# Performance work log

Hardware: AMD Instinct MI355X
Metric: run time of the kernel (lower is better)

## Reference

```python
import jax, jax.numpy as jnp
import numpy as np

B, T, D = 2, 1024, 1024
H, DH = 16, 64          # d_head = d_model // n_heads
MAX_POS = 64


def setup_inputs() -> dict:
    key = jax.random.key(0)
    ks = jax.random.split(key, 11)
    s = 1.0 / np.sqrt(D)
    x = jax.random.normal(ks[0], (B, T, D), jnp.float32)
    Wq = jax.random.normal(ks[1], (D, D), jnp.float32) * s
    Wk = jax.random.normal(ks[2], (D, D), jnp.float32) * s
    Wv = jax.random.normal(ks[3], (D, D), jnp.float32) * s
    Wo = jax.random.normal(ks[4], (D, D), jnp.float32) * s
    bq = jnp.zeros((D,), jnp.float32)
    bk = jnp.zeros((D,), jnp.float32)
    bv = jnp.zeros((D,), jnp.float32)
    bo = jnp.zeros((D,), jnp.float32)
    pos_emb = jax.random.normal(ks[5], (H, MAX_POS, DH), jnp.float32) * 0.02
    causal_mask = jnp.triu(jnp.ones((T, T), bool), k=1)  # True = masked (j > i)
    return dict(x=x, Wq=Wq, bq=bq, Wk=Wk, bk=bk, Wv=Wv, bv=bv, Wo=Wo, bo=bo,
                pos_emb=pos_emb, causal_mask=causal_mask)


def reference(x, Wq, bq, Wk, bk, Wv, bv, Wo, bo, pos_emb, causal_mask):
    Bv, Tv, _ = x.shape
    scale = np.sqrt(DH).astype(np.float32)

    def proj(W, b):
        return (x @ W.T + b).reshape(Bv, Tv, H, DH).transpose(0, 2, 1, 3)  # (B,H,T,d)

    Q, K, V = proj(Wq, bq), proj(Wk, bk), proj(Wv, bv)

    qk = jnp.einsum('bhid,bhjd->bhij', Q, K)              # (B,H,T,T)
    gates = jax.nn.sigmoid(qk / scale)
    gates = jnp.where(causal_mask, 0.0, gates)
    cum = jnp.cumsum(gates, axis=-1)
    pos = cum[..., -1:] - cum                             # total - cumsum_left

    pos = jnp.clip(pos, 0.0, MAX_POS - 1.0)
    pos_floor = jnp.floor(pos)
    alpha = (pos - pos_floor)[..., None]                  # (B,H,T,T,1) -> broadcast
    fidx = pos_floor.astype(jnp.int32)
    cidx = jnp.clip(jnp.ceil(pos), 0, MAX_POS - 1).astype(jnp.int32)

    # q_i . PE_{i,j} via precomputed q.pos_emb table (same math, no (B,H,T,T,d) tensor)
    qpe_tab = jnp.einsum('bhid,hpd->bhip', Q, pos_emb)    # (B,H,T,MAX_POS)
    qpe_f = jnp.take_along_axis(qpe_tab, fidx, axis=-1)   # (B,H,T,T)
    qpe_c = jnp.take_along_axis(qpe_tab, cidx, axis=-1)
    q_pe = (1.0 - alpha[..., 0]) * qpe_f + alpha[..., 0] * qpe_c

    scores = (qk + q_pe) / scale
    scores = jnp.where(causal_mask, -jnp.inf, scores)
    attn = jax.nn.softmax(scores, axis=-1)

    out = jnp.einsum('bhij,bhjd->bhid', attn, V)
    out = out.transpose(0, 2, 1, 3).reshape(Bv, Tv, D)
    return out @ Wo.T + bo
```

## Files before the change

kernel.cpp:

```cpp
#include <hip/hip_runtime.h>
#include <math.h>

#define Tt 1024
#define Dd 1024
#define Hh 16
#define DHh 64
#define MAXPOS 64
#define BTt 2048

typedef short short8 __attribute__((ext_vector_type(8)));
typedef float floatx4 __attribute__((ext_vector_type(4)));

#define MFMA16 __builtin_amdgcn_mfma_f32_16x16x32_bf16

__device__ __forceinline__ unsigned short f2bf(float f) {
    unsigned u;
    __builtin_memcpy(&u, &f, 4);
    u = (u + 0x7FFFu + ((u >> 16) & 1u)) >> 16;
    return (unsigned short)u;
}
__device__ __forceinline__ float bf2fs(short s) {
    unsigned u = ((unsigned)(unsigned short)s) << 16;
    float f;
    __builtin_memcpy(&f, &u, 4);
    return f;
}
__device__ __forceinline__ float fsigm(float x) {
    return __builtin_amdgcn_rcpf(1.f + __expf(-x));
}
__device__ __forceinline__ void gl2lds16(const short* __restrict__ g, short* l) {
    __builtin_amdgcn_global_load_lds(
        (const __attribute__((address_space(1))) void*)g,
        (__attribute__((address_space(3))) void*)l,
        16, 0, 0);
}

__global__ __launch_bounds__(256) void conv_bf16(
    const float* __restrict__ x,  const float* __restrict__ W0,
    const float* __restrict__ W1, const float* __restrict__ W2,
    const float* __restrict__ W3,
    short* __restrict__ xb, short* __restrict__ w0b, short* __restrict__ w1b,
    short* __restrict__ w2b, short* __restrict__ w3b)
{
    const float* src; short* dst; int n;
    switch (blockIdx.y) {
        case 0:  src = x;  dst = xb;  n = BTt * Dd; break;
        case 1:  src = W0; dst = w0b; n = Dd * Dd;  break;
        case 2:  src = W1; dst = w1b; n = Dd * Dd;  break;
        case 3:  src = W2; dst = w2b; n = Dd * Dd;  break;
        default: src = W3; dst = w3b; n = Dd * Dd;  break;
    }
    int idx = (blockIdx.x * 256 + threadIdx.x) * 8;
    if (idx >= n) return;
    floatx4 a0 = *(const floatx4*)&src[idx];
    floatx4 a1 = *(const floatx4*)&src[idx + 4];
    short8 s;
    for (int e = 0; e < 4; ++e) {
        s[e]     = (short)f2bf(a0[e]);
        s[e + 4] = (short)f2bf(a1[e]);
    }
    *(short8*)&dst[idx] = s;
}

template <int MODE, int TMW>
__device__ __forceinline__ void gemm_body(const short* __restrict__ A,
                                          const short* __restrict__ W,
                                          const float* __restrict__ bias,
                                          void* __restrict__ Cout,
                                          int N, int K)
{
    __shared__ __align__(16) short Ash[2][TMW * 64 * 64];
    __shared__ __align__(16) short Bsh[2][64 * 64];
    const int t = threadIdx.x;
    const int lane = t & 63, wave = t >> 6;
    const int quad = lane >> 4, l16 = lane & 15;
    const int row0 = blockIdx.x * (TMW * 64), col0 = blockIdx.y * 64;

    const int g_r = lane >> 3, g_c = (lane & 7) * 8;

    floatx4 acc[TMW][4];
    for (int a = 0; a < TMW; ++a)
        for (int b2 = 0; b2 < 4; ++b2)
            acc[a][b2] = (floatx4){0.f, 0.f, 0.f, 0.f};

#define STAGE(buf, kb)                                                      \
    do {                                                                    \
        for (int i = 0; i < TMW * 2; ++i) {                                 \
            int rbase = (wave * (TMW * 2) + i) * 8;                         \
            gl2lds16(&A[(size_t)(row0 + rbase + g_r) * K + (kb) + g_c],     \
                     &Ash[buf][rbase * 64]);                                \
        }                                                                   \
        for (int i = 0; i < 2; ++i) {                                       \
            int rbase = (wave * 2 + i) * 8;                                 \
            gl2lds16(&W[(size_t)(col0 + rbase + g_r) * K + (kb) + g_c],     \
                     &Bsh[buf][rbase * 64]);                                \
        }                                                                   \
    } while (0)

    const int NT = K / 64;
    STAGE(0, 0);
    __syncthreads();
    for (int ts = 0; ts < NT; ++ts) {
        const int cur = ts & 1;
        if (ts + 1 < NT) STAGE(cur ^ 1, (ts + 1) * 64);
        for (int ks = 0; ks < 2; ++ks) {
            short8 af[TMW], bfr[4];
            for (int tm = 0; tm < TMW; ++tm)
                af[tm] = *(short8*)&Ash[cur][(wave * (TMW * 16) + tm * 16 + l16) * 64 + ks * 32 + quad * 8];
            for (int tn = 0; tn < 4; ++tn)
                bfr[tn] = *(short8*)&Bsh[cur][(tn * 16 + l16) * 64 + ks * 32 + quad * 8];
            for (int tm = 0; tm < TMW; ++tm)
                for (int tn = 0; tn < 4; ++tn)
                    acc[tm][tn] = MFMA16(af[tm], bfr[tn], acc[tm][tn], 0, 0, 0);
        }
        if (ts + 1 < NT) __syncthreads();
    }
#undef STAGE
    for (int tm = 0; tm < TMW; ++tm)
        for (int tn = 0; tn < 4; ++tn) {
            int col = col0 + tn * 16 + l16;
            float bv = bias[col];
            for (int r = 0; r < 4; ++r) {
                int row = row0 + wave * (TMW * 16) + tm * 16 + quad * 4 + r;
                float v = acc[tm][tn][r] + bv;
                if (MODE == 0) ((float*)Cout)[(size_t)row * N + col] = v;
                else           ((short*)Cout)[(size_t)row * N + col] = (short)f2bf(v);
            }
        }
}

__global__ __launch_bounds__(256) void gemm_qkv(
    const short* __restrict__ xb,
    const short* __restrict__ Wqb, const short* __restrict__ Wkb,
    const short* __restrict__ Wvb,
    const float* __restrict__ bq, const float* __restrict__ bk,
    const float* __restrict__ bv,
    short* __restrict__ Qb, short* __restrict__ Kb, short* __restrict__ Vrow)
{
    if (blockIdx.z == 0)      gemm_body<1, 2>(xb, Wqb, bq, Qb, Dd, Dd);
    else if (blockIdx.z == 1) gemm_body<1, 2>(xb, Wkb, bk, Kb, Dd, Dd);
    else                      gemm_body<1, 2>(xb, Wvb, bv, Vrow, Dd, Dd);
}

__global__ __launch_bounds__(256) void gemm_o(
    const short* __restrict__ A, const short* __restrict__ W,
    const float* __restrict__ bias, float* __restrict__ C)
{
    gemm_body<0, 1>(A, W, bias, C, Dd, Dd);
}

__global__ __launch_bounds__(256) void v_transpose(
    const short* __restrict__ Vrow, short* __restrict__ Vt)
{
    __shared__ __align__(16) short L[64 * 72];
    const int t = threadIdx.x;
    const int j0 = blockIdx.x * 64, d0 = blockIdx.y * 64, b = blockIdx.z;
    for (int s = 0; s < 2; ++s) {
        int c = t * 2 + s;
        int jr = c >> 3, c8 = c & 7;
        *(short8*)&L[jr * 72 + c8 * 8] =
            *(const short8*)&Vrow[((size_t)(b * Tt + j0 + jr)) * Dd + d0 + c8 * 8];
    }
    __syncthreads();
    for (int s = 0; s < 2; ++s) {
        int c = t * 2 + s;
        int dr = c >> 3, c8 = c & 7;
        short8 v;
        for (int e = 0; e < 8; ++e) v[e] = L[(c8 * 8 + e) * 72 + dr];
        *(short8*)&Vt[((size_t)(b * Dd + d0 + dr)) * Tt + j0 + c8 * 8] = v;
    }
}

__global__ __launch_bounds__(256) void cope_attn(
    const short* __restrict__ Q, const short* __restrict__ K,
    const short* __restrict__ Vt, const float* __restrict__ PE,
    short* __restrict__ AOb)
{
    const int h = blockIdx.y, b = blockIdx.z;
    const int t = threadIdx.x, lane = t & 63, wave = t >> 6;
    const int quad = lane >> 4, l16 = lane & 15;

    __shared__ __align__(16) short SldS[32 * 264];
    __shared__ __align__(16) short KV[128 * 72];
    __shared__ short qpeB[32 * 68];
    __shared__ float lrow[32];
    float* Sld = (float*)SldS;

    const float inv_scale = 0.125f;
    const int sr = t >> 3, ss = t & 7;

    for (int phase = 0; phase < 2; ++phase) {
        const int it = (phase == 0) ? (31 - (int)blockIdx.x) : (int)blockIdx.x;
        const int i0 = it * 32;
        const int irow = i0 + sr;

        short* QtS = SldS;
        {
            int r = t >> 3, c = t & 7;
            *(short8*)&QtS[r * 72 + c * 8] =
                *(const short8*)&Q[((size_t)(b * Tt + i0 + r)) * Dd + h * DHh + c * 8];
        }
        for (int e = 0; e < 16; ++e) {
            int idx = t + 256 * e;
            int p = idx >> 6, d = idx & 63;
            KV[p * 72 + d] = (short)f2bf(PE[((size_t)h * MAXPOS + p) * DHh + d]);
        }
        __syncthreads();

        short8 qa[2][2];
        for (int rb = 0; rb < 2; ++rb)
            for (int ks = 0; ks < 2; ++ks)
                qa[rb][ks] = *(short8*)&QtS[(rb * 16 + l16) * 72 + ks * 32 + quad * 8];

        {
            int mt = wave >> 1;
            int ntA = 2 * (wave & 1), ntB = ntA + 1;
            floatx4 c0f = {0, 0, 0, 0}, c1f = {0, 0, 0, 0};
            for (int ks = 0; ks < 2; ++ks) {
                short8 b0 = *(short8*)&KV[(ntA * 16 + l16) * 72 + ks * 32 + quad * 8];
                short8 b1 = *(short8*)&KV[(ntB * 16 + l16) * 72 + ks * 32 + quad * 8];
                c0f = MFMA16(qa[mt][ks], b0, c0f, 0, 0, 0);
                c1f = MFMA16(qa[mt][ks], b1, c1f, 0, 0, 0);
            }
            for (int r = 0; r < 4; ++r) {
                qpeB[(mt * 16 + quad * 4 + r) * 68 + ntA * 16 + l16] = (short)f2bf(c0f[r]);
                qpeB[(mt * 16 + quad * 4 + r) * 68 + ntB * 16 + l16] = (short)f2bf(c1f[r]);
            }
        }

        const int JT = (i0 + 159) >> 7;
        floatx4 o0 = {0, 0, 0, 0}, o1 = {0, 0, 0, 0};
        const int pv_mt = wave >> 1;
        const int pv_ntA = 2 * (wave & 1), pv_ntB = pv_ntA + 1;
        float l_acc = 0.f;
        float rightAcc = 0.f;

        short8 kreg[4];
        for (int e = 0; e < 4; ++e) {
            int ch = t + 256 * e;
            int jr = ch >> 3, c = ch & 7;
            kreg[e] = *(const short8*)&K[((size_t)(b * Tt + (JT - 1) * 128 + jr)) * Dd + h * DHh + c * 8];
        }

        for (int jt = JT - 1; jt >= 0; --jt) {
            const int j0 = jt * 128;
            __syncthreads();
            for (int e = 0; e < 4; ++e) {
                int ch = t + 256 * e;
                int jr = ch >> 3, c = ch & 7;
                *(short8*)&KV[jr * 72 + c * 8] = kreg[e];
            }
            __syncthreads();
            {
                int ntA = 2 * wave, ntB = ntA + 1;
                floatx4 c00 = {0,0,0,0}, c01 = {0,0,0,0}, c10 = {0,0,0,0}, c11 = {0,0,0,0};
                for (int ks = 0; ks < 2; ++ks) {
                    short8 b0 = *(short8*)&KV[(ntA * 16 + l16) * 72 + ks * 32 + quad * 8];
                    short8 b1 = *(short8*)&KV[(ntB * 16 + l16) * 72 + ks * 32 + quad * 8];
                    c00 = MFMA16(qa[0][ks], b0, c00, 0, 0, 0);
                    c01 = MFMA16(qa[0][ks], b1, c01, 0, 0, 0);
                    c10 = MFMA16(qa[1][ks], b0, c10, 0, 0, 0);
                    c11 = MFMA16(qa[1][ks], b1, c11, 0, 0, 0);
                }
                for (int r = 0; r < 4; ++r) {
                    Sld[(quad * 4 + r) * 132 + ntA * 16 + l16] = c00[r];
                    Sld[(quad * 4 + r) * 132 + ntB * 16 + l16] = c01[r];
                    Sld[(16 + quad * 4 + r) * 132 + ntA * 16 + l16] = c10[r];
                    Sld[(16 + quad * 4 + r) * 132 + ntB * 16 + l16] = c11[r];
                }
            }
            __syncthreads();
            short8 vreg[4];
            for (int e = 0; e < 4; ++e) {
                int ch = t + 256 * e;
                int d = ch >> 4, c = ch & 15;
                vreg[e] = *(const short8*)&Vt[((size_t)(b * Dd + h * DHh + d)) * Tt + j0 + c * 8];
            }
            if (jt > 0) {
                for (int e = 0; e < 4; ++e) {
                    int ch = t + 256 * e;
                    int jr = ch >> 3, c = ch & 7;
                    kreg[e] = *(const short8*)&K[((size_t)(b * Tt + j0 - 128 + jr)) * Dd + h * DHh + c * 8];
                }
            }
            {
                floatx4 qv[4];
                for (int q4 = 0; q4 < 4; ++q4) {
                    short8 qraw = *(short8*)&SldS[sr * 264 + ss * 32 + q4 * 8];
                    __builtin_memcpy(&qv[q4], &qraw, 16);
                }
                float gt[16];
                float gs = 0.f;
                for (int e = 0; e < 16; ++e) {
                    int j = j0 + ss * 16 + e;
                    float qk = qv[e >> 2][e & 3];
                    float g = (j <= irow) ? fsigm(qk * inv_scale) : 0.f;
                    gt[e] = g;
                    gs += g;
                }
                float inc = gs;
                for (int d2 = 1; d2 < 8; d2 <<= 1) {
                    float n = __shfl_down(inc, d2, 64);
                    if ((lane & 7) + d2 < 8) inc += n;
                }
                float tileTot = __shfl(inc, lane & 56, 64);
                float base = rightAcc + (inc - gs);
                float run = 0.f;
                short8 p0, p1;
                for (int e = 15; e >= 0; --e) {
                    int j = j0 + ss * 16 + e;
                    float pos = base + run;
                    run += gt[e];
                    pos = fminf(fmaxf(pos, 0.f), 63.f);
                    float pf = floorf(pos);
                    float al = pos - pf;
                    int fi = (int)pf;
                    int ci = fi + 1; if (ci > 63) ci = 63;
                    float qp = (1.f - al) * bf2fs(qpeB[sr * 68 + fi]) + al * bf2fs(qpeB[sr * 68 + ci]);
                    float qk = qv[e >> 2][e & 3];
                    float p = (j <= irow) ? __expf((qk + qp) * inv_scale) : 0.f;
                    if (e < 8) p0[e] = (short)f2bf(p); else p1[e - 8] = (short)f2bf(p);
                    l_acc += p;
                }
                *(short8*)&SldS[sr * 264 + ss * 32]     = p0;
                *(short8*)&SldS[sr * 264 + ss * 32 + 8] = p1;
                rightAcc += tileTot;
            }
            for (int e = 0; e < 4; ++e) {
                int ch = t + 256 * e;
                int d = ch >> 4, c = ch & 15;
                *(short8*)&KV[d * 136 + c * 8] = vreg[e];
            }
            __syncthreads();
            for (int ks = 0; ks < 4; ++ks) {
                short8 a  = *(short8*)&SldS[(pv_mt * 16 + l16) * 264 + ks * 64
                                            + ((quad >> 1) << 5) + ((quad & 1) << 3)];
                short8 b0 = *(short8*)&KV[(pv_ntA * 16 + l16) * 136 + ks * 32 + quad * 8];
                short8 b1 = *(short8*)&KV[(pv_ntB * 16 + l16) * 136 + ks * 32 + quad * 8];
                o0 = MFMA16(a, b0, o0, 0, 0, 0);
                o1 = MFMA16(a, b1, o1, 0, 0, 0);
            }
        }
        float lr = l_acc;
        for (int d2 = 4; d2 >= 1; d2 >>= 1) lr += __shfl_xor(lr, d2, 64);
        if (ss == 0) lrow[sr] = lr;
        __syncthreads();
        for (int r = 0; r < 4; ++r) {
            int row = pv_mt * 16 + quad * 4 + r;
            float inv = __builtin_amdgcn_rcpf(lrow[row]);
            size_t off = ((size_t)(b * Tt + i0 + row)) * Dd + h * DHh;
            AOb[off + pv_ntA * 16 + l16] = (short)f2bf(o0[r] * inv);
            AOb[off + pv_ntB * 16 + l16] = (short)f2bf(o1[r] * inv);
        }
    }
}

extern "C" void kernel_launch(void* const* d_in, const int* in_sizes, int n_in,
                              void* d_out, int out_size, void* d_ws, size_t ws_size,
                              hipStream_t stream)
{
    const float* x  = (const float*)d_in[0];
    const float* Wq = (const float*)d_in[1];
    const float* bq = (const float*)d_in[2];
    const float* Wk = (const float*)d_in[3];
    const float* bk = (const float*)d_in[4];
    const float* Wv = (const float*)d_in[5];
    const float* bv = (const float*)d_in[6];
    const float* Wo = (const float*)d_in[7];
    const float* bo = (const float*)d_in[8];
    const float* pe = (const float*)d_in[9];

    short* xb   = (short*)d_ws;
    short* Wqb  = xb   + (size_t)BTt * Dd;
    short* Wkb  = Wqb  + (size_t)Dd * Dd;
    short* Wvb  = Wkb  + (size_t)Dd * Dd;
    short* Wob  = Wvb  + (size_t)Dd * Dd;
    short* Qb   = Wob  + (size_t)Dd * Dd;
    short* Kb   = Qb   + (size_t)BTt * Dd;
    short* Vrow = Kb   + (size_t)BTt * Dd;
    short* Vtg  = Vrow + (size_t)BTt * Dd;
    short* AOb  = Vtg  + (size_t)BTt * Dd;

    dim3 gc(BTt * Dd / 8 / 256, 5);
    conv_bf16<<<gc, 256, 0, stream>>>(x, Wq, Wk, Wv, Wo, xb, Wqb, Wkb, Wvb, Wob);

    dim3 gq(BTt / 128, Dd / 64, 3);
    gemm_qkv<<<gq, 256, 0, stream>>>(xb, Wqb, Wkb, Wvb, bq, bk, bv, Qb, Kb, Vrow);

    dim3 gv(Tt / 64, Dd / 64, 2);
    v_transpose<<<gv, 256, 0, stream>>>(Vrow, Vtg);

    dim3 ga(Tt / 32 / 2, Hh, 2);
    cope_attn<<<ga, 256, 0, stream>>>(Qb, Kb, Vtg, pe, AOb);

    dim3 go(BTt / 64, Dd / 64, 1);
    gemm_o<<<go, 256, 0, stream>>>(AOb, Wob, bo, (float*)d_out);
}
```

Before: 178.7 us.

## Fuse V transpose into QKV GEMM epilogue and precompute qpe interpolation pairs

New measurement: 192.8 us. +7.9%, slower.

```diff
diff --git a/kernel.cpp b/kernel.cpp
--- a/kernel.cpp
+++ b/kernel.cpp
@@ -10,6 +10,7 @@
 
 typedef short short8 __attribute__((ext_vector_type(8)));
 typedef float floatx4 __attribute__((ext_vector_type(4)));
+typedef float floatx2 __attribute__((ext_vector_type(2)));
 
 #define MFMA16 __builtin_amdgcn_mfma_f32_16x16x32_bf16
 
@@ -123,8 +124,12 @@
             for (int r = 0; r < 4; ++r) {
                 int row = row0 + wave * (TMW * 16) + tm * 16 + quad * 4 + r;
                 float v = acc[tm][tn][r] + bv;
-                if (MODE == 0) ((float*)Cout)[(size_t)row * N + col] = v;
-                else           ((short*)Cout)[(size_t)row * N + col] = (short)f2bf(v);
+                if (MODE == 0)      ((float*)Cout)[(size_t)row * N + col] = v;
+                else if (MODE == 1) ((short*)Cout)[(size_t)row * N + col] = (short)f2bf(v);
+                else {
+                    int bi = row >> 10, j = row & (Tt - 1);
+                    ((short*)Cout)[((size_t)(bi * Dd + col)) * Tt + j] = (short)f2bf(v);
+                }
             }
         }
 }
@@ -135,11 +140,11 @@
     const short* __restrict__ Wvb,
     const float* __restrict__ bq, const float* __restrict__ bk,
     const float* __restrict__ bv,
-    short* __restrict__ Qb, short* __restrict__ Kb, short* __restrict__ Vrow)
+    short* __restrict__ Qb, short* __restrict__ Kb, short* __restrict__ Vt)
 {
     if (blockIdx.z == 0)      gemm_body<1, 2>(xb, Wqb, bq, Qb, Dd, Dd);
     else if (blockIdx.z == 1) gemm_body<1, 2>(xb, Wkb, bk, Kb, Dd, Dd);
-    else                      gemm_body<1, 2>(xb, Wvb, bv, Vrow, Dd, Dd);
+    else                      gemm_body<2, 2>(xb, Wvb, bv, Vt, Dd, Dd);
 }
 
 __global__ __launch_bounds__(256) void gemm_o(
@@ -147,28 +152,6 @@
     const float* __restrict__ bias, float* __restrict__ C)
 {
     gemm_body<0, 1>(A, W, bias, C, Dd, Dd);
-}
-
-__global__ __launch_bounds__(256) void v_transpose(
-    const short* __restrict__ Vrow, short* __restrict__ Vt)
-{
-    __shared__ __align__(16) short L[64 * 72];
-    const int t = threadIdx.x;
-    const int j0 = blockIdx.x * 64, d0 = blockIdx.y * 64, b = blockIdx.z;
-    for (int s = 0; s < 2; ++s) {
-        int c = t * 2 + s;
-        int jr = c >> 3, c8 = c & 7;
-        *(short8*)&L[jr * 72 + c8 * 8] =
-            *(const short8*)&Vrow[((size_t)(b * Tt + j0 + jr)) * Dd + d0 + c8 * 8];
-    }
-    __syncthreads();
-    for (int s = 0; s < 2; ++s) {
-        int c = t * 2 + s;
-        int dr = c >> 3, c8 = c & 7;
-        short8 v;
-        for (int e = 0; e < 8; ++e) v[e] = L[(c8 * 8 + e) * 72 + dr];
-        *(short8*)&Vt[((size_t)(b * Dd + d0 + dr)) * Tt + j0 + c8 * 8] = v;
-    }
 }
 
 __global__ __launch_bounds__(256) void cope_attn(
@@ -182,7 +165,7 @@
 
     __shared__ __align__(16) short SldS[32 * 264];
     __shared__ __align__(16) short KV[128 * 72];
-    __shared__ short qpeB[32 * 68];
+    __shared__ floatx2 qpeP[32 * 64];
     __shared__ float lrow[32];
     float* Sld = (float*)SldS;
 
@@ -212,6 +195,7 @@
             for (int ks = 0; ks < 2; ++ks)
                 qa[rb][ks] = *(short8*)&QtS[(rb * 16 + l16) * 72 + ks * 32 + quad * 8];
 
+        float* qsc = (float*)&SldS[2304];
         {
             int mt = wave >> 1;
             int ntA = 2 * (wave & 1), ntB = ntA + 1;
@@ -223,8 +207,21 @@
                 c1f = MFMA16(qa[mt][ks], b1, c1f, 0, 0, 0);
             }
             for (int r = 0; r < 4; ++r) {
-                qpeB[(mt * 16 + quad * 4 + r) * 68 + ntA * 16 + l16] = (short)f2bf(c0f[r]);
-                qpeB[(mt * 16 + quad * 4 + r) * 68 + ntB * 16 + l16] = (short)f2bf(c1f[r]);
+                qsc[(mt * 16 + quad * 4 + r) * 64 + ntA * 16 + l16] = c0f[r];
+                qsc[(mt * 16 + quad * 4 + r) * 64 + ntB * 16 + l16] = c1f[r];
+            }
+        }
+        __syncthreads();
+        {
+            int base = t * 8;
+            for (int k = 0; k < 8; ++k) {
+                int idx = base + k;
+                int cc = idx & 63;
+                float v0 = qsc[idx];
+                float v1 = (cc < 63) ? qsc[idx + 1] : v0;
+                v0 = bf2fs((short)f2bf(v0));
+                v1 = bf2fs((short)f2bf(v1));
+                qpeP[idx] = (floatx2){v0, v1 - v0};
             }
         }
 
@@ -315,8 +312,8 @@
                     float pf = floorf(pos);
                     float al = pos - pf;
                     int fi = (int)pf;
-                    int ci = fi + 1; if (ci > 63) ci = 63;
-                    float qp = (1.f - al) * bf2fs(qpeB[sr * 68 + fi]) + al * bf2fs(qpeB[sr * 68 + ci]);
+                    floatx2 pr = qpeP[sr * 64 + fi];
+                    float qp = pr.x + al * pr.y;
                     float qk = qv[e >> 2][e & 3];
                     float p = (j <= irow) ? __expf((qk + qp) * inv_scale) : 0.f;
                     if (e < 8) p0[e] = (short)f2bf(p); else p1[e - 8] = (short)f2bf(p);
@@ -377,18 +374,14 @@
     short* Wob  = Wvb  + (size_t)Dd * Dd;
     short* Qb   = Wob  + (size_t)Dd * Dd;
     short* Kb   = Qb   + (size_t)BTt * Dd;
-    short* Vrow = Kb   + (size_t)BTt * Dd;
-    short* Vtg  = Vrow + (size_t)BTt * Dd;
+    short* Vtg  = Kb   + (size_t)BTt * Dd;
     short* AOb  = Vtg  + (size_t)BTt * Dd;
 
     dim3 gc(BTt * Dd / 8 / 256, 5);
     conv_bf16<<<gc, 256, 0, stream>>>(x, Wq, Wk, Wv, Wo, xb, Wqb, Wkb, Wvb, Wob);
 
     dim3 gq(BTt / 128, Dd / 64, 3);
-    gemm_qkv<<<gq, 256, 0, stream>>>(xb, Wqb, Wkb, Wvb, bq, bk, bv, Qb, Kb, Vrow);
-
-    dim3 gv(Tt / 64, Dd / 64, 2);
-    v_transpose<<<gv, 256, 0, stream>>>(Vrow, Vtg);
+    gemm_qkv<<<gq, 256, 0, stream>>>(xb, Wqb, Wkb, Wvb, bq, bk, bv, Qb, Kb, Vtg);
 
     dim3 ga(Tt / 32 / 2, Hh, 2);
     cope_attn<<<ga, 256, 0, stream>>>(Qb, Kb, Vtg, pe, AOb);
```

## Halve attention query tile to 16 rows, doubling blocks, and pack qpe lerp table

Applied to the files above, without the earlier changes.

Result: no change. 181.8 us (+1.7%).

```diff
diff --git a/kernel.cpp b/kernel.cpp
--- a/kernel.cpp
+++ b/kernel.cpp
@@ -10,6 +10,7 @@
 
 typedef short short8 __attribute__((ext_vector_type(8)));
 typedef float floatx4 __attribute__((ext_vector_type(4)));
+typedef float floatx2 __attribute__((ext_vector_type(2)));
 
 #define MFMA16 __builtin_amdgcn_mfma_f32_16x16x32_bf16
 
@@ -180,22 +181,22 @@
     const int t = threadIdx.x, lane = t & 63, wave = t >> 6;
     const int quad = lane >> 4, l16 = lane & 15;
 
-    __shared__ __align__(16) short SldS[32 * 264];
+    __shared__ __align__(16) short SldS[16 * 264];
     __shared__ __align__(16) short KV[128 * 72];
-    __shared__ short qpeB[32 * 68];
-    __shared__ float lrow[32];
+    __shared__ floatx2 qpeP[16 * 64];
+    __shared__ float lrow[16];
     float* Sld = (float*)SldS;
 
     const float inv_scale = 0.125f;
-    const int sr = t >> 3, ss = t & 7;
+    const int sr = t >> 4, ss = t & 15;
 
     for (int phase = 0; phase < 2; ++phase) {
-        const int it = (phase == 0) ? (31 - (int)blockIdx.x) : (int)blockIdx.x;
-        const int i0 = it * 32;
+        const int it = (phase == 0) ? (63 - (int)blockIdx.x) : (int)blockIdx.x;
+        const int i0 = it * 16;
         const int irow = i0 + sr;
 
         short* QtS = SldS;
-        {
+        if (t < 128) {
             int r = t >> 3, c = t & 7;
             *(short8*)&QtS[r * 72 + c * 8] =
                 *(const short8*)&Q[((size_t)(b * Tt + i0 + r)) * Dd + h * DHh + c * 8];
@@ -207,31 +208,36 @@
         }
         __syncthreads();
 
-        short8 qa[2][2];
-        for (int rb = 0; rb < 2; ++rb)
-            for (int ks = 0; ks < 2; ++ks)
-                qa[rb][ks] = *(short8*)&QtS[(rb * 16 + l16) * 72 + ks * 32 + quad * 8];
-
+        short8 qa[2];
+        for (int ks = 0; ks < 2; ++ks)
+            qa[ks] = *(short8*)&QtS[l16 * 72 + ks * 32 + quad * 8];
+
+        float* qsc = (float*)&KV[64 * 72];
         {
-            int mt = wave >> 1;
-            int ntA = 2 * (wave & 1), ntB = ntA + 1;
-            floatx4 c0f = {0, 0, 0, 0}, c1f = {0, 0, 0, 0};
+            floatx4 c0f = {0, 0, 0, 0};
             for (int ks = 0; ks < 2; ++ks) {
-                short8 b0 = *(short8*)&KV[(ntA * 16 + l16) * 72 + ks * 32 + quad * 8];
-                short8 b1 = *(short8*)&KV[(ntB * 16 + l16) * 72 + ks * 32 + quad * 8];
-                c0f = MFMA16(qa[mt][ks], b0, c0f, 0, 0, 0);
-                c1f = MFMA16(qa[mt][ks], b1, c1f, 0, 0, 0);
-            }
-            for (int r = 0; r < 4; ++r) {
-                qpeB[(mt * 16 + quad * 4 + r) * 68 + ntA * 16 + l16] = (short)f2bf(c0f[r]);
-                qpeB[(mt * 16 + quad * 4 + r) * 68 + ntB * 16 + l16] = (short)f2bf(c1f[r]);
-            }
-        }
-
-        const int JT = (i0 + 159) >> 7;
-        floatx4 o0 = {0, 0, 0, 0}, o1 = {0, 0, 0, 0};
-        const int pv_mt = wave >> 1;
-        const int pv_ntA = 2 * (wave & 1), pv_ntB = pv_ntA + 1;
+                short8 b0 = *(short8*)&KV[(wave * 16 + l16) * 72 + ks * 32 + quad * 8];
+                c0f = MFMA16(qa[ks], b0, c0f, 0, 0, 0);
+            }
+            __syncthreads();
+            for (int r = 0; r < 4; ++r)
+                qsc[(quad * 4 + r) * 64 + wave * 16 + l16] = c0f[r];
+        }
+        __syncthreads();
+        {
+            for (int k = 0; k < 4; ++k) {
+                int idx = t * 4 + k;
+                int cc = idx & 63;
+                float v0 = qsc[idx];
+                float v1 = (cc < 63) ? qsc[idx + 1] : v0;
+                v0 = bf2fs((short)f2bf(v0));
+                v1 = bf2fs((short)f2bf(v1));
+                qpeP[idx] = (floatx2){v0, v1 - v0};
+            }
+        }
+
+        const int JT = (it >> 3) + 1;
+        floatx4 o0 = {0, 0, 0, 0};
         float l_acc = 0.f;
         float rightAcc = 0.f;
 
@@ -253,20 +259,16 @@
             __syncthreads();
             {
                 int ntA = 2 * wave, ntB = ntA + 1;
-                floatx4 c00 = {0,0,0,0}, c01 = {0,0,0,0}, c10 = {0,0,0,0}, c11 = {0,0,0,0};
+                floatx4 c00 = {0,0,0,0}, c01 = {0,0,0,0};
                 for (int ks = 0; ks < 2; ++ks) {
                     short8 b0 = *(short8*)&KV[(ntA * 16 + l16) * 72 + ks * 32 + quad * 8];
                     short8 b1 = *(short8*)&KV[(ntB * 16 + l16) * 72 + ks * 32 + quad * 8];
-                    c00 = MFMA16(qa[0][ks], b0, c00, 0, 0, 0);
-                    c01 = MFMA16(qa[0][ks], b1, c01, 0, 0, 0);
-                    c10 = MFMA16(qa[1][ks], b0, c10, 0, 0, 0);
-                    c11 = MFMA16(qa[1][ks], b1, c11, 0, 0, 0);
+                    c00 = MFMA16(qa[ks], b0, c00, 0, 0, 0);
+                    c01 = MFMA16(qa[ks], b1, c01, 0, 0, 0);
                 }
                 for (int r = 0; r < 4; ++r) {
                     Sld[(quad * 4 + r) * 132 + ntA * 16 + l16] = c00[r];
                     Sld[(quad * 4 + r) * 132 + ntB * 16 + l16] = c01[r];
-                    Sld[(16 + quad * 4 + r) * 132 + ntA * 16 + l16] = c10[r];
-                    Sld[(16 + quad * 4 + r) * 132 + ntB * 16 + l16] = c11[r];
                 }
             }
             __syncthreads();
@@ -284,46 +286,45 @@
                 }
             }
             {
-                floatx4 qv[4];
-                for (int q4 = 0; q4 < 4; ++q4) {
-                    short8 qraw = *(short8*)&SldS[sr * 264 + ss * 32 + q4 * 8];
+                floatx4 qv[2];
+                for (int q4 = 0; q4 < 2; ++q4) {
+                    short8 qraw = *(short8*)&SldS[sr * 264 + ss * 16 + q4 * 8];
                     __builtin_memcpy(&qv[q4], &qraw, 16);
                 }
-                float gt[16];
+                float gt[8];
                 float gs = 0.f;
-                for (int e = 0; e < 16; ++e) {
-                    int j = j0 + ss * 16 + e;
+                for (int e = 0; e < 8; ++e) {
+                    int j = j0 + ss * 8 + e;
                     float qk = qv[e >> 2][e & 3];
                     float g = (j <= irow) ? fsigm(qk * inv_scale) : 0.f;
                     gt[e] = g;
                     gs += g;
                 }
                 float inc = gs;
-                for (int d2 = 1; d2 < 8; d2 <<= 1) {
+                for (int d2 = 1; d2 < 16; d2 <<= 1) {
                     float n = __shfl_down(inc, d2, 64);
-                    if ((lane & 7) + d2 < 8) inc += n;
-                }
-                float tileTot = __shfl(inc, lane & 56, 64);
+                    if ((lane & 15) + d2 < 16) inc += n;
+                }
+                float tileTot = __shfl(inc, lane & 48, 64);
                 float base = rightAcc + (inc - gs);
                 float run = 0.f;
-                short8 p0, p1;
-                for (int e = 15; e >= 0; --e) {
-                    int j = j0 + ss * 16 + e;
+                short8 p0;
+                for (int e = 7; e >= 0; --e) {
+                    int j = j0 + ss * 8 + e;
                     float pos = base + run;
                     run += gt[e];
                     pos = fminf(fmaxf(pos, 0.f), 63.f);
                     float pf = floorf(pos);
                     float al = pos - pf;
                     int fi = (int)pf;
-                    int ci = fi + 1; if (ci > 63) ci = 63;
-                    float qp = (1.f - al) * bf2fs(qpeB[sr * 68 + fi]) + al * bf2fs(qpeB[sr * 68 + ci]);
+                    floatx2 pr = qpeP[sr * 64 + fi];
+                    float qp = pr.x + al * pr.y;
                     float qk = qv[e >> 2][e & 3];
                     float p = (j <= irow) ? __expf((qk + qp) * inv_scale) : 0.f;
-                    if (e < 8) p0[e] = (short)f2bf(p); else p1[e - 8] = (short)f2bf(p);
+                    p0[e] = (short)f2bf(p);
                     l_acc += p;
                 }
-                *(short8*)&SldS[sr * 264 + ss * 32]     = p0;
-                *(short8*)&SldS[sr * 264 + ss * 32 + 8] = p1;
+                *(short8*)&SldS[sr * 264 + ss * 16] = p0;
                 rightAcc += tileTot;
             }
             for (int e = 0; e < 4; ++e) {
@@ -333,25 +334,22 @@
             }
             __syncthreads();
             for (int ks = 0; ks < 4; ++ks) {
-                short8 a  = *(short8*)&SldS[(pv_mt * 16 + l16) * 264 + ks * 64
-                                            + ((quad >> 1) << 5) + ((quad & 1) << 3)];
-                short8 b0 = *(short8*)&KV[(pv_ntA * 16 + l16) * 136 + ks * 32 + quad * 8];
-                short8 b1 = *(short8*)&KV[(pv_ntB * 16 + l16) * 136 + ks * 32 + quad * 8];
+                short8 a  = *(short8*)&SldS[l16 * 264 + (ks * 4 + quad) * 16];
+                short8 b0 = *(short8*)&KV[(wave * 16 + l16) * 136 + ks * 32 + quad * 8];
                 o0 = MFMA16(a, b0, o0, 0, 0, 0);
-                o1 = MFMA16(a, b1, o1, 0, 0, 0);
             }
         }
         float lr = l_acc;
-        for (int d2 = 4; d2 >= 1; d2 >>= 1) lr += __shfl_xor(lr, d2, 64);
+        for (int d2 = 8; d2 >= 1; d2 >>= 1) lr += __shfl_xor(lr, d2, 64);
         if (ss == 0) lrow[sr] = lr;
         __syncthreads();
         for (int r = 0; r < 4; ++r) {
-            int row = pv_mt * 16 + quad * 4 + r;
+            int row = quad * 4 + r;
             float inv = __builtin_amdgcn_rcpf(lrow[row]);
             size_t off = ((size_t)(b * Tt + i0 + row)) * Dd + h * DHh;
-            AOb[off + pv_ntA * 16 + l16] = (short)f2bf(o0[r] * inv);
-            AOb[off + pv_ntB * 16 + l16] = (short)f2bf(o1[r] * inv);
-        }
+            AOb[off + wave * 16 + l16] = (short)f2bf(o0[r] * inv);
+        }
+        __syncthreads();
     }
 }
 
@@ -390,7 +388,7 @@
     dim3 gv(Tt / 64, Dd / 64, 2);
     v_transpose<<<gv, 256, 0, stream>>>(Vrow, Vtg);
 
-    dim3 ga(Tt / 32 / 2, Hh, 2);
+    dim3 ga(Tt / 16 / 2, Hh, 2);
     cope_attn<<<ga, 256, 0, stream>>>(Qb, Kb, Vtg, pe, AOb);
 
     dim3 go(BTt / 64, Dd / 64, 1);
```
